# Performance work log

Measured on AMD Instinct MI355X. Metric: run time of the kernel, lower is better.

## Reference

```python
import jax, jax.numpy as jnp
import numpy as np

S, N, H = 1024, 64, 1024  # source len, batch, hidden_size
INPUT_SIZE = 1024         # attention projection dim (linear1/linear2 out)


def setup_inputs() -> dict:
    key = jax.random.key(0)
    ks = jax.random.split(key, 8)
    sc_h = 1.0 / np.sqrt(H)
    sc_i = 1.0 / np.sqrt(INPUT_SIZE)
    return {
        "out_e": jax.random.normal(ks[0], (S, N, H), dtype=jnp.float32),
        "hidden_d": jax.random.normal(ks[1], (1, N, H), dtype=jnp.float32),
        # torch Linear weights are [out_features, in_features]
        "W1": jax.random.uniform(ks[2], (INPUT_SIZE, H), jnp.float32, -sc_h, sc_h),
        "b1": jax.random.uniform(ks[3], (INPUT_SIZE,), jnp.float32, -sc_h, sc_h),
        "W2": jax.random.uniform(ks[4], (INPUT_SIZE, H), jnp.float32, -sc_h, sc_h),
        "b2": jax.random.uniform(ks[5], (INPUT_SIZE,), jnp.float32, -sc_h, sc_h),
        "W3": jax.random.uniform(ks[6], (1, INPUT_SIZE), jnp.float32, -sc_i, sc_i),
        "b3": jax.random.uniform(ks[7], (1,), jnp.float32, -sc_i, sc_i),
    }


def reference(out_e, hidden_d, W1, b1, W2, b2, W3, b3):
    # hidden_d [1,N,H] broadcast to [S,N,H] (torch .repeat)
    s = out_e.shape[0]
    hd = jnp.broadcast_to(hidden_d, (s,) + hidden_d.shape[1:])
    # a: [S,N,1] = linear3(tanh(linear1(hd) + linear2(out_e)))
    e = jnp.tanh(hd @ W1.T + b1 + out_e @ W2.T + b2)
    a = e @ W3.T + b3
    # softmax over the source dim (dim=0 in torch)
    alpha = jax.nn.softmax(a, axis=0)          # [S,N,1]
    c = jnp.einsum('sne,snh->enh', alpha, out_e)  # [1,N,H]
    return (c, alpha)
```

## Files before the change

### kernel.cpp

```cpp
#include <hip/hip_runtime.h>
#include <hip/hip_fp16.h>

#define S_LEN 1024
#define N_B   64
#define H_DIM 1024
#define I_DIM 1024
#define M_ROWS (S_LEN * N_B)

typedef __attribute__((ext_vector_type(8))) _Float16 half8;
typedef __attribute__((ext_vector_type(4))) _Float16 half4;
typedef __attribute__((ext_vector_type(4))) float    f32x4;

__device__ __forceinline__ void gload16(const void* g, void* l) {
  __builtin_amdgcn_global_load_lds(
      (const __attribute__((address_space(1))) unsigned int*)g,
      (__attribute__((address_space(3))) unsigned int*)l, 16, 0, 0);
}

__global__ void cvt_f32_f16(const float* __restrict__ src,
                            _Float16* __restrict__ dst, int n4) {
  int idx = blockIdx.x * blockDim.x + threadIdx.x;
  int stride = gridDim.x * blockDim.x;
  const float4* s4 = (const float4*)src;
  half4* d4 = (half4*)dst;
  for (int i = idx; i < n4; i += stride) {
    float4 v = s4[i];
    half4 h;
    h[0] = (_Float16)v.x; h[1] = (_Float16)v.y;
    h[2] = (_Float16)v.z; h[3] = (_Float16)v.w;
    d4[i] = h;
  }
}

__global__ void u1_kernel(const float* __restrict__ hd,
                          const float* __restrict__ W1,
                          const float* __restrict__ b1,
                          const float* __restrict__ b2,
                          float* __restrict__ u1) {
  __shared__ float hs[4 * 1024];
  int nb = blockIdx.x & 15;
  int ib = blockIdx.x >> 4;
  int t = threadIdx.x;
  int n0 = nb * 4;

  const float4* g4 = (const float4*)(hd + (size_t)n0 * 1024);
  float4* h4 = (float4*)hs;
#pragma unroll
  for (int r = 0; r < 4; ++r) h4[r * 256 + t] = g4[r * 256 + t];
  __syncthreads();

  int il = t >> 2, q = t & 3;
  int i = ib * 64 + il;
  const float4* w4 = (const float4*)(W1 + (size_t)i * 1024 + q * 256);
  float s0 = 0.f, s1 = 0.f, s2 = 0.f, s3 = 0.f;
  for (int hh = 0; hh < 64; ++hh) {
    float4 wv = w4[hh];
    int hb = q * 256 + hh * 4;
    float4 v0 = *(const float4*)&hs[0 * 1024 + hb];
    float4 v1 = *(const float4*)&hs[1 * 1024 + hb];
    float4 v2 = *(const float4*)&hs[2 * 1024 + hb];
    float4 v3 = *(const float4*)&hs[3 * 1024 + hb];
    s0 += wv.x * v0.x + wv.y * v0.y + wv.z * v0.z + wv.w * v0.w;
    s1 += wv.x * v1.x + wv.y * v1.y + wv.z * v1.z + wv.w * v1.w;
    s2 += wv.x * v2.x + wv.y * v2.y + wv.z * v2.z + wv.w * v2.w;
    s3 += wv.x * v3.x + wv.y * v3.y + wv.z * v3.z + wv.w * v3.w;
  }
  s0 += __shfl_xor(s0, 1); s0 += __shfl_xor(s0, 2);
  s1 += __shfl_xor(s1, 1); s1 += __shfl_xor(s1, 2);
  s2 += __shfl_xor(s2, 1); s2 += __shfl_xor(s2, 2);
  s3 += __shfl_xor(s3, 1); s3 += __shfl_xor(s3, 2);
  if (q == 0) {
    float bb = b1[i] + b2[i];
    u1[(size_t)(n0 + 0) * 1024 + i] = s0 + bb;
    u1[(size_t)(n0 + 1) * 1024 + i] = s1 + bb;
    u1[(size_t)(n0 + 2) * 1024 + i] = s2 + bb;
    u1[(size_t)(n0 + 3) * 1024 + i] = s3 + bb;
  }
}

__global__ __launch_bounds__(256) void fused_gemm_tanh(
    const _Float16* __restrict__ A,
    const _Float16* __restrict__ B,
    const float* __restrict__ u1,
    const float* __restrict__ W3,
    float* __restrict__ a_ws)
{
  __shared__ __align__(16) _Float16 As[2][128 * 32];
  __shared__ __align__(16) _Float16 Bs[2][128 * 32];

  const int t = threadIdx.x;
  const int lane = t & 63;
  const int w = t >> 6;
  const int wr = w >> 1, wc = w & 1;
  const int bx = blockIdx.x;
  const int xcd = bx & 7;
  const int j = bx >> 3;
  const int rb = xcd + ((j >> 3) << 3);
  const int cb = j & 7;
  const int m0 = rb * 128, i0 = cb * 128;

  const int strow = t >> 2;
  const int stcol = (t & 3) * 8;
  const _Float16* gA = A + (size_t)(m0 + strow) * 1024 + stcol;
  const _Float16* gB = B + (size_t)(i0 + strow) * 1024 + stcol;
  const int ldsoff = strow * 32 + stcol;

  f32x4 acc[4][4] = {};

  gload16(gA,             &As[0][ldsoff]);
  gload16(gA + 64 * 1024, &As[0][ldsoff + 64 * 32]);
  gload16(gB,             &Bs[0][ldsoff]);
  gload16(gB + 64 * 1024, &Bs[0][ldsoff + 64 * 32]);
  __syncthreads();

  const int fr = lane & 15;
  const int kg = lane >> 4;
  const int aoff = (wr * 64 + fr) * 32 + kg * 8;
  const int boff = (wc * 64 + fr) * 32 + kg * 8;

  for (int kt = 0; kt < 32; ++kt) {
    const int buf = kt & 1;
    if (kt < 31) {
      const _Float16* gA2 = gA + (kt + 1) * 32;
      const _Float16* gB2 = gB + (kt + 1) * 32;
      gload16(gA2,             &As[buf ^ 1][ldsoff]);
      gload16(gA2 + 64 * 1024, &As[buf ^ 1][ldsoff + 64 * 32]);
      gload16(gB2,             &Bs[buf ^ 1][ldsoff]);
      gload16(gB2 + 64 * 1024, &Bs[buf ^ 1][ldsoff + 64 * 32]);
    }
    half8 af[4], bf[4];
#pragma unroll
    for (int mi = 0; mi < 4; ++mi)
      af[mi] = *(const half8*)&As[buf][aoff + mi * 16 * 32];
#pragma unroll
    for (int ni = 0; ni < 4; ++ni)
      bf[ni] = *(const half8*)&Bs[buf][boff + ni * 16 * 32];
#pragma unroll
    for (int mi = 0; mi < 4; ++mi)
#pragma unroll
      for (int ni = 0; ni < 4; ++ni)
        acc[mi][ni] = __builtin_amdgcn_mfma_f32_16x16x32_f16(
            af[mi], bf[ni], acc[mi][ni], 0, 0, 0);
    __syncthreads();
  }

  float w3v[4];
#pragma unroll
  for (int ni = 0; ni < 4; ++ni)
    w3v[ni] = W3[i0 + wc * 64 + ni * 16 + fr];

#pragma unroll
  for (int mi = 0; mi < 4; ++mi) {
#pragma unroll
    for (int jj = 0; jj < 4; ++jj) {
      int m = m0 + wr * 64 + mi * 16 + kg * 4 + jj;
      int n = m & 63;
      const float* u1row = u1 + (size_t)n * 1024 + i0 + wc * 64;
      float s = 0.f;
#pragma unroll
      for (int ni = 0; ni < 4; ++ni) {
        float e = acc[mi][ni][jj] + u1row[ni * 16 + fr];
        float th = 1.f - 2.f / (__expf(2.f * e) + 1.f);
        s += th * w3v[ni];
      }
      s += __shfl_xor(s, 1);
      s += __shfl_xor(s, 2);
      s += __shfl_xor(s, 4);
      s += __shfl_xor(s, 8);
      if (fr == 0) atomicAdd(&a_ws[m], s);
    }
  }
}

__global__ void softmax_col(const float* __restrict__ a_ws,
                            float* __restrict__ alpha) {
  int n = blockIdx.x;
  int t = threadIdx.x;
  __shared__ float red[256];
  float v[4];
  float mx = -1e30f;
#pragma unroll
  for (int q = 0; q < 4; ++q) {
    v[q] = a_ws[(size_t)(t + q * 256) * 64 + n];
    mx = fmaxf(mx, v[q]);
  }
  red[t] = mx; __syncthreads();
  for (int off = 128; off > 0; off >>= 1) {
    if (t < off) red[t] = fmaxf(red[t], red[t + off]);
    __syncthreads();
  }
  mx = red[0];
  __syncthreads();
  float sum = 0.f;
#pragma unroll
  for (int q = 0; q < 4; ++q) { v[q] = __expf(v[q] - mx); sum += v[q]; }
  red[t] = sum; __syncthreads();
  for (int off = 128; off > 0; off >>= 1) {
    if (t < off) red[t] += red[t + off];
    __syncthreads();
  }
  float inv = 1.f / red[0];
#pragma unroll
  for (int q = 0; q < 4; ++q)
    alpha[(size_t)(t + q * 256) * 64 + n] = v[q] * inv;
}

__global__ void weighted_sum(const _Float16* __restrict__ oe,
                             const float* __restrict__ alpha,
                             float* __restrict__ cout) {
  int n = blockIdx.x & 63;
  int sc = blockIdx.x >> 6;
  int t = threadIdx.x;
  __shared__ float al[64];
  if (t < 64) al[t] = alpha[(size_t)(sc * 64 + t) * 64 + n];
  __syncthreads();
  float a0 = 0.f, a1 = 0.f, a2 = 0.f, a3 = 0.f;
#pragma unroll 4
  for (int sl = 0; sl < 64; ++sl) {
    float a = al[sl];
    int s = sc * 64 + sl;
    half4 x = *(const half4*)(oe + (size_t)(s * 64 + n) * 1024 + t * 4);
    a0 += a * (float)x[0]; a1 += a * (float)x[1];
    a2 += a * (float)x[2]; a3 += a * (float)x[3];
  }
  float* c = cout + (size_t)n * 1024 + t * 4;
  atomicAdd(c + 0, a0);
  atomicAdd(c + 1, a1);
  atomicAdd(c + 2, a2);
  atomicAdd(c + 3, a3);
}

extern "C" void kernel_launch(void* const* d_in, const int* in_sizes, int n_in,
                              void* d_out, int out_size, void* d_ws,
                              size_t ws_size, hipStream_t stream) {
  const float* out_e    = (const float*)d_in[0];
  const float* hidden_d = (const float*)d_in[1];
  const float* W1       = (const float*)d_in[2];
  const float* b1       = (const float*)d_in[3];
  const float* W2       = (const float*)d_in[4];
  const float* b2       = (const float*)d_in[5];
  const float* W3       = (const float*)d_in[6];

  char* ws = (char*)d_ws;
  _Float16* oe16 = (_Float16*)ws;
  _Float16* w216 = (_Float16*)(ws + 134217728);
  float* u1   = (float*)(ws + 134217728 + 2097152);
  float* a_ws = (float*)(ws + 134217728 + 2097152 + 262144);

  float* c_out = (float*)d_out;
  float* alpha = (float*)d_out + 65536;

  hipLaunchKernelGGL(cvt_f32_f16, dim3(2048), dim3(256), 0, stream,
                     out_e, oe16, 67108864 / 4);
  hipLaunchKernelGGL(cvt_f32_f16, dim3(256), dim3(256), 0, stream,
                     W2, w216, 1048576 / 4);
  hipLaunchKernelGGL(u1_kernel, dim3(256), dim3(256), 0, stream,
                     hidden_d, W1, b1, b2, u1);
  hipMemsetAsync(a_ws, 0, 65536 * 4, stream);
  hipMemsetAsync(c_out, 0, 65536 * 4, stream);
  hipLaunchKernelGGL(fused_gemm_tanh, dim3(4096), dim3(256), 0, stream,
                     oe16, w216, u1, W3, a_ws);
  hipLaunchKernelGGL(softmax_col, dim3(64), dim3(256), 0, stream,
                     a_ws, alpha);
  hipLaunchKernelGGL(weighted_sum, dim3(1024), dim3(256), 0, stream,
                     oe16, alpha, c_out);
}
```

Before: 655.0 us.

## Enlarge GEMM tile to 256x256 with prefetch-ahead pipeline and wider conversion

The fused GEMM+tanh kernel moves from 128x128 tiles with 4 waves to 256x256 tiles with 8 waves, each wave computing 128x64. Larger tiles cut global and LDS traffic per FLOP. The K loop now issues loads two stages ahead using explicit vmcnt waits and raw barriers instead of __syncthreads, and raises wave priority around the MFMA blocks. The fp32-to-fp16 conversion kernel now writes 8 halves per thread. In exchange, register pressure from 32 accumulators and the doubled LDS use may lower occupancy.

```diff
diff --git a/kernel.cpp b/kernel.cpp
--- a/kernel.cpp
+++ b/kernel.cpp
@@ -5,7 +5,6 @@
 #define N_B   64
 #define H_DIM 1024
 #define I_DIM 1024
-#define M_ROWS (S_LEN * N_B)
 
 typedef __attribute__((ext_vector_type(8))) _Float16 half8;
 typedef __attribute__((ext_vector_type(4))) _Float16 half4;
@@ -18,17 +17,19 @@
 }
 
 __global__ void cvt_f32_f16(const float* __restrict__ src,
-                            _Float16* __restrict__ dst, int n4) {
+                            _Float16* __restrict__ dst, int n8) {
   int idx = blockIdx.x * blockDim.x + threadIdx.x;
   int stride = gridDim.x * blockDim.x;
   const float4* s4 = (const float4*)src;
-  half4* d4 = (half4*)dst;
-  for (int i = idx; i < n4; i += stride) {
-    float4 v = s4[i];
-    half4 h;
-    h[0] = (_Float16)v.x; h[1] = (_Float16)v.y;
-    h[2] = (_Float16)v.z; h[3] = (_Float16)v.w;
-    d4[i] = h;
+  half8* d8 = (half8*)dst;
+  for (int i = idx; i < n8; i += stride) {
+    float4 a = s4[2 * i], b = s4[2 * i + 1];
+    half8 h;
+    h[0] = (_Float16)a.x; h[1] = (_Float16)a.y;
+    h[2] = (_Float16)a.z; h[3] = (_Float16)a.w;
+    h[4] = (_Float16)b.x; h[5] = (_Float16)b.y;
+    h[6] = (_Float16)b.z; h[7] = (_Float16)b.w;
+    d8[i] = h;
   }
 }
 
@@ -78,88 +79,100 @@
   }
 }
 
-__global__ __launch_bounds__(256) void fused_gemm_tanh(
+__global__ __launch_bounds__(512) void fused_gemm_tanh(
     const _Float16* __restrict__ A,
     const _Float16* __restrict__ B,
     const float* __restrict__ u1,
     const float* __restrict__ W3,
     float* __restrict__ a_ws)
 {
-  __shared__ __align__(16) _Float16 As[2][128 * 32];
-  __shared__ __align__(16) _Float16 Bs[2][128 * 32];
+  __shared__ __align__(16) _Float16 As[2][256 * 32];
+  __shared__ __align__(16) _Float16 Bs[2][256 * 32];
 
   const int t = threadIdx.x;
   const int lane = t & 63;
   const int w = t >> 6;
-  const int wr = w >> 1, wc = w & 1;
+  const int wr = w >> 2, wc = w & 3;
   const int bx = blockIdx.x;
   const int xcd = bx & 7;
   const int j = bx >> 3;
-  const int rb = xcd + ((j >> 3) << 3);
-  const int cb = j & 7;
-  const int m0 = rb * 128, i0 = cb * 128;
-
-  const int strow = t >> 2;
-  const int stcol = (t & 3) * 8;
-  const _Float16* gA = A + (size_t)(m0 + strow) * 1024 + stcol;
-  const _Float16* gB = B + (size_t)(i0 + strow) * 1024 + stcol;
-  const int ldsoff = strow * 32 + stcol;
-
-  f32x4 acc[4][4] = {};
-
-  gload16(gA,             &As[0][ldsoff]);
-  gload16(gA + 64 * 1024, &As[0][ldsoff + 64 * 32]);
-  gload16(gB,             &Bs[0][ldsoff]);
-  gload16(gB + 64 * 1024, &Bs[0][ldsoff + 64 * 32]);
-  __syncthreads();
+  const int rb = xcd + ((j >> 2) << 3);
+  const int cb = j & 3;
+  const int m0 = rb * 256, i0 = cb * 256;
 
   const int fr = lane & 15;
   const int kg = lane >> 4;
-  const int aoff = (wr * 64 + fr) * 32 + kg * 8;
+
+  const int srow = t >> 2, sunit = t & 3;
+  const _Float16* gA = A + (size_t)(m0 + srow) * 1024 + sunit * 8;
+  const _Float16* gB = B + (size_t)(i0 + srow) * 1024 + sunit * 8;
+  const int ldst = t * 8;
+
+#define STAGE(kt) do { int b2 = (kt) & 1; int kc = (kt) * 32;       \
+    gload16(gA + kc,               &As[b2][ldst]);                   \
+    gload16(gA + kc + 128 * 1024,  &As[b2][ldst + 4096]);            \
+    gload16(gB + kc,               &Bs[b2][ldst]);                   \
+    gload16(gB + kc + 128 * 1024,  &Bs[b2][ldst + 4096]); } while (0)
+
+  f32x4 acc[8][4] = {};
+
+  STAGE(0);
+  STAGE(1);
+
+  const int aoff = (wr * 128 + fr) * 32 + kg * 8;
   const int boff = (wc * 64 + fr) * 32 + kg * 8;
 
   for (int kt = 0; kt < 32; ++kt) {
-    const int buf = kt & 1;
-    if (kt < 31) {
-      const _Float16* gA2 = gA + (kt + 1) * 32;
-      const _Float16* gB2 = gB + (kt + 1) * 32;
-      gload16(gA2,             &As[buf ^ 1][ldsoff]);
-      gload16(gA2 + 64 * 1024, &As[buf ^ 1][ldsoff + 64 * 32]);
-      gload16(gB2,             &Bs[buf ^ 1][ldsoff]);
-      gload16(gB2 + 64 * 1024, &Bs[buf ^ 1][ldsoff + 64 * 32]);
+    const int b = kt & 1;
+    if (kt == 31)
+      asm volatile("s_waitcnt vmcnt(0)" ::: "memory");
+    else
+      asm volatile("s_waitcnt vmcnt(4)" ::: "memory");
+    __builtin_amdgcn_s_barrier();
+    asm volatile("" ::: "memory");
+
+    half8 bf[4];
+#pragma unroll
+    for (int ni = 0; ni < 4; ++ni)
+      bf[ni] = *(const half8*)&Bs[b][boff + ni * 512];
+#pragma unroll
+    for (int mh = 0; mh < 2; ++mh) {
+      half8 af[4];
+#pragma unroll
+      for (int mi = 0; mi < 4; ++mi)
+        af[mi] = *(const half8*)&As[b][aoff + (mh * 4 + mi) * 512];
+      __builtin_amdgcn_s_setprio(1);
+#pragma unroll
+      for (int mi = 0; mi < 4; ++mi)
+#pragma unroll
+        for (int ni = 0; ni < 4; ++ni)
+          acc[mh * 4 + mi][ni] = __builtin_amdgcn_mfma_f32_16x16x32_f16(
+              af[mi], bf[ni], acc[mh * 4 + mi][ni], 0, 0, 0);
+      __builtin_amdgcn_s_setprio(0);
     }
-    half8 af[4], bf[4];
-#pragma unroll
-    for (int mi = 0; mi < 4; ++mi)
-      af[mi] = *(const half8*)&As[buf][aoff + mi * 16 * 32];
-#pragma unroll
-    for (int ni = 0; ni < 4; ++ni)
-      bf[ni] = *(const half8*)&Bs[buf][boff + ni * 16 * 32];
-#pragma unroll
-    for (int mi = 0; mi < 4; ++mi)
-#pragma unroll
-      for (int ni = 0; ni < 4; ++ni)
-        acc[mi][ni] = __builtin_amdgcn_mfma_f32_16x16x32_f16(
-            af[mi], bf[ni], acc[mi][ni], 0, 0, 0);
-    __syncthreads();
-  }
+    asm volatile("s_waitcnt lgkmcnt(0)" ::: "memory");
+    __builtin_amdgcn_s_barrier();
+    asm volatile("" ::: "memory");
+    if (kt < 30) STAGE(kt + 2);
+  }
+#undef STAGE
 
   float w3v[4];
 #pragma unroll
   for (int ni = 0; ni < 4; ++ni)
     w3v[ni] = W3[i0 + wc * 64 + ni * 16 + fr];
-
-#pragma unroll
-  for (int mi = 0; mi < 4; ++mi) {
+  const float* u1base = u1 + i0 + wc * 64 + fr;
+
+#pragma unroll
+  for (int mi = 0; mi < 8; ++mi) {
 #pragma unroll
     for (int jj = 0; jj < 4; ++jj) {
-      int m = m0 + wr * 64 + mi * 16 + kg * 4 + jj;
-      int n = m & 63;
-      const float* u1row = u1 + (size_t)n * 1024 + i0 + wc * 64;
+      int m = m0 + wr * 128 + mi * 16 + kg * 4 + jj;
+      const float* u1row = u1base + (size_t)(m & 63) * 1024;
       float s = 0.f;
 #pragma unroll
       for (int ni = 0; ni < 4; ++ni) {
-        float e = acc[mi][ni][jj] + u1row[ni * 16 + fr];
+        float e = acc[mi][ni][jj] + u1row[ni * 16];
         float th = 1.f - 2.f / (__expf(2.f * e) + 1.f);
         s += th * w3v[ni];
       }
@@ -251,14 +264,14 @@
   float* alpha = (float*)d_out + 65536;
 
   hipLaunchKernelGGL(cvt_f32_f16, dim3(2048), dim3(256), 0, stream,
-                     out_e, oe16, 67108864 / 4);
-  hipLaunchKernelGGL(cvt_f32_f16, dim3(256), dim3(256), 0, stream,
-                     W2, w216, 1048576 / 4);
+                     out_e, oe16, 67108864 / 8);
+  hipLaunchKernelGGL(cvt_f32_f16, dim3(512), dim3(256), 0, stream,
+                     W2, w216, 1048576 / 8);
   hipLaunchKernelGGL(u1_kernel, dim3(256), dim3(256), 0, stream,
                      hidden_d, W1, b1, b2, u1);
   hipMemsetAsync(a_ws, 0, 65536 * 4, stream);
   hipMemsetAsync(c_out, 0, 65536 * 4, stream);
-  hipLaunchKernelGGL(fused_gemm_tanh, dim3(4096), dim3(256), 0, stream,
+  hipLaunchKernelGGL(fused_gemm_tanh, dim3(1024), dim3(512), 0, stream,
                      oe16, w216, u1, W3, a_ws);
   hipLaunchKernelGGL(softmax_col, dim3(64), dim3(256), 0, stream,
                      a_ws, alpha);
```

After: 681.4 us. 4.0% more time.
